# Performance work log

Measured on AMD Instinct MI355X. Metric: run time of the kernel, lower is better.

Reference implementation:

```python
import jax, jax.numpy as jnp
import numpy as np
import math

B, S, D = 8, 1024, 1024
NH, NKV, HD = 16, 8, 64
BLK_NUM, BLK_SIZE = 128, 8

def apply_rope(x, cos, sin):
    # x: (B,S,H,HD); cos/sin: (S, HD//2)
    x1 = x[..., 0::2]
    x2 = x[..., 1::2]
    c = cos[None, :, None, :]
    s = sin[None, :, None, :]
    r1 = x1 * c - x2 * s
    r2 = x1 * s + x2 * c
    out = jnp.stack([r1, r2], axis=-1).reshape(x.shape)
    return out

def setup_inputs() -> dict:
    key = jax.random.key(0)
    ks = jax.random.split(key, 7)
    x = jax.random.normal(ks[0], (B, S, D), dtype=jnp.float32)
    scale = 1.0 / math.sqrt(D)
    wq = jax.random.normal(ks[1], (D, NH * HD), dtype=jnp.float32) * scale
    wk = jax.random.normal(ks[2], (D, NKV * HD), dtype=jnp.float32) * scale
    wv = jax.random.normal(ks[3], (D, NKV * HD), dtype=jnp.float32) * scale
    wo = jax.random.normal(ks[4], (NH * HD, D), dtype=jnp.float32) * scale
    pos = jnp.arange(S, dtype=jnp.float32)
    inv_freq = 1.0 / (10000.0 ** (jnp.arange(0, HD, 2, dtype=jnp.float32) / HD))
    ang = pos[:, None] * inv_freq[None, :]
    freqs_cis_cos = jnp.cos(ang)
    freqs_cis_sin = jnp.sin(ang)
    return {"x": x, "wq": wq, "wk": wk, "wv": wv, "wo": wo,
            "freqs_cis_cos": freqs_cis_cos, "freqs_cis_sin": freqs_cis_sin,
            "start_pos": 0}

def reference(x, wq, wk, wv, wo, freqs_cis_cos, freqs_cis_sin, start_pos):
    q = (x @ wq).reshape(B, S, NH, HD)
    k = (x @ wk).reshape(B, S, NKV, HD)
    v = (x @ wv).reshape(B, S, NKV, HD)
    q = apply_rope(q, freqs_cis_cos, freqs_cis_sin)
    k = apply_rope(k, freqs_cis_cos, freqs_cis_sin)
    # GQA: repeat kv heads
    rep = NH // NKV
    k = jnp.repeat(k, rep, axis=2)  # (B,S,NH,HD)
    v = jnp.repeat(v, rep, axis=2)
    # block-causal mask: q in block i attends to kv blocks j <= i
    blk_id = jnp.arange(S) // BLK_SIZE
    mask = blk_id[:, None] >= blk_id[None, :]  # (S,S)
    scores = jnp.einsum('bqhd,bkhd->bhqk', q, k) / math.sqrt(HD)
    scores = jnp.where(mask[None, None], scores, -jnp.inf)
    attn = jax.nn.softmax(scores, axis=-1)
    out = jnp.einsum('bhqk,bkhd->bqhd', attn, v).reshape(B, S, NH * HD)
    return out @ wo
```

## Files before the change

### kernel.cpp

```cpp
#include <hip/hip_runtime.h>
#include <cstdint>
#include <math.h>

#define B_   8
#define S_   1024
#define D_   1024
#define NH_  16
#define NKV_ 8
#define HD_  64
#define M_   (B_*S_)

using bf16   = __bf16;
using bf16x4 = __attribute__((ext_vector_type(4))) __bf16;
using bf16x8 = __attribute__((ext_vector_type(8))) __bf16;
using f32x4  = __attribute__((ext_vector_type(4))) float;

__device__ __forceinline__ void gll16(const bf16* g, const bf16* l) {
    __builtin_amdgcn_global_load_lds(
        (const __attribute__((address_space(1))) unsigned int*)(uintptr_t)g,
        (__attribute__((address_space(3))) unsigned int*)(uintptr_t)l,
        16, 0, 0);
}

__device__ __forceinline__ void vm_wait0()  { asm volatile("s_waitcnt vmcnt(0)" ::: "memory"); }
__device__ __forceinline__ void bar()       { __builtin_amdgcn_s_barrier(); asm volatile("" ::: "memory"); }

__global__ void k_prep1(const float* __restrict__ x,
                        const float* __restrict__ wq, const float* __restrict__ wk,
                        const float* __restrict__ wv, const float* __restrict__ wo,
                        bf16* __restrict__ xb, bf16* __restrict__ wqkvT, bf16* __restrict__ woT) {
    __shared__ float tile[64 * 65];
    int bid = blockIdx.x;
    int t = threadIdx.x;
    if (bid < 8192) {
        int i = bid * 256 + t;
        float4 v = ((const float4*)x)[i];
        bf16x4 o = { (bf16)v.x, (bf16)v.y, (bf16)v.z, (bf16)v.w };
        ((bf16x4*)xb)[i] = o;
        return;
    }
    int b2 = bid - 8192;
    int bx = b2 % 48, by = b2 / 48;
    const int R = 1024;
    const float* in; bf16* out; int C, xo;
    if (bx < 16)      { in = wq; out = wqkvT;               C = 1024; xo = bx; }
    else if (bx < 24) { in = wk; out = wqkvT + 1024 * 1024; C = 512;  xo = bx - 16; }
    else if (bx < 32) { in = wv; out = wqkvT + 1536 * 1024; C = 512;  xo = bx - 24; }
    else              { in = wo; out = woT;                 C = 1024; xo = bx - 32; }
    int r0 = by * 64, c0 = xo * 64;
    #pragma unroll
    for (int it = 0; it < 16; ++it) {
        int idx = it * 256 + t;
        int r = idx >> 6, c = idx & 63;
        tile[r * 65 + c] = in[(size_t)(r0 + r) * C + c0 + c];
    }
    __syncthreads();
    #pragma unroll
    for (int it = 0; it < 16; ++it) {
        int idx = it * 256 + t;
        int c = idx >> 6, r = idx & 63;
        out[(size_t)(c0 + c) * R + r0 + r] = (bf16)tile[r * 65 + c];
    }
}

template <typename OutT, int BN>
__global__ __launch_bounds__(512, 2) void k_gemm256(const bf16* __restrict__ A,
                                                    const bf16* __restrict__ Bt,
                                                    OutT* __restrict__ C, int M, int N, int K) {
    constexpr int NI = BN / 64;
    constexpr int NB = (BN * 8) / 512;
    __shared__ __align__(16) bf16 aLds[2 * 256 * 64];
    __shared__ __align__(16) bf16 bLds[2 * BN * 64];
    const int t    = threadIdx.x;
    const int lane = t & 63;
    const int w    = t >> 6;
    const int quad = lane >> 4;
    const int l16  = lane & 15;
    const int wr   = w >> 2;
    const int wc   = w & 3;

    int bid = blockIdx.y * gridDim.x + blockIdx.x;
    int cpx = (gridDim.x * gridDim.y) >> 3;
    int sw  = (bid & 7) * cpx + (bid >> 3);
    int bx  = sw % gridDim.x, by = sw / gridDim.x;
    const int m0 = by * 256;
    const int n0 = bx * BN;

    f32x4 acc[8][NI] = {};

    auto stageA = [&](int kb, int buf) {
        const int k0 = kb << 6;
        #pragma unroll
        for (int it = 0; it < 4; ++it) {
            int ci = it * 512 + t;
            int r = ci >> 3, c = ci & 7;
            int cg = c ^ (r & 7);
            gll16(A + (size_t)(m0 + r) * K + k0 + cg * 8, aLds + buf * (256 * 64) + ci * 8);
        }
    };
    auto stageB = [&](int kb, int buf) {
        const int k0 = kb << 6;
        #pragma unroll
        for (int it = 0; it < NB; ++it) {
            int ci = it * 512 + t;
            int r = ci >> 3, c = ci & 7;
            int cg = c ^ (r & 7);
            gll16(Bt + (size_t)(n0 + r) * K + k0 + cg * 8, bLds + buf * (BN * 64) + ci * 8);
        }
    };

    const int NT = K >> 6;

    auto phase = [&](int buf, int kk, int mh, int stageSel, int nkb, bool lastInTile) {
        const bf16* aL = aLds + buf * (256 * 64);
        const bf16* bL = bLds + buf * (BN * 64);
        bf16x8 af[4], bfr[NI];
        #pragma unroll
        for (int i = 0; i < 4; ++i) {
            int row = wr * 128 + (mh * 4 + i) * 16 + l16;
            int ch  = (kk * 4 + quad) ^ (row & 7);
            af[i] = *(const bf16x8*)&aL[row * 64 + ch * 8];
        }
        #pragma unroll
        for (int ni = 0; ni < NI; ++ni) {
            int row = wc * (NI * 16) + ni * 16 + l16;
            int ch  = (kk * 4 + quad) ^ (row & 7);
            bfr[ni] = *(const bf16x8*)&bL[row * 64 + ch * 8];
        }
        if (stageSel == 1) stageA(nkb, buf ^ 1);
        else if (stageSel == 2) stageB(nkb, buf ^ 1);
        bar();
        __builtin_amdgcn_s_setprio(1);
        #pragma unroll
        for (int i = 0; i < 4; ++i)
            #pragma unroll
            for (int ni = 0; ni < NI; ++ni)
                acc[mh * 4 + i][ni] = __builtin_amdgcn_mfma_f32_16x16x32_bf16(af[i], bfr[ni], acc[mh * 4 + i][ni], 0, 0, 0);
        __builtin_amdgcn_s_setprio(0);
        if (lastInTile) vm_wait0();
        bar();
    };

    auto doTile = [&](int T, int buf) {
        bool hn = (T + 1 < NT);
        phase(buf, 0, 0, hn ? 1 : 0, T + 1, false);
        phase(buf, 0, 1, hn ? 2 : 0, T + 1, false);
        phase(buf, 1, 0, 0, 0, false);
        phase(buf, 1, 1, 0, 0, true);
    };

    stageA(0, 0); stageB(0, 0);
    vm_wait0();
    bar();
    for (int T = 0; T < NT; T += 2) {
        doTile(T, 0);
        doTile(T + 1, 1);
    }

    #pragma unroll
    for (int mi = 0; mi < 8; ++mi)
        #pragma unroll
        for (int ni = 0; ni < NI; ++ni)
            #pragma unroll
            for (int r = 0; r < 4; ++r) {
                int row = m0 + wr * 128 + mi * 16 + quad * 4 + r;
                int col = n0 + wc * (NI * 16) + ni * 16 + l16;
                C[(size_t)row * N + col] = (OutT)acc[mi][ni][r];
            }
}

__global__ void k_prep2(const bf16* __restrict__ qkv, const float* __restrict__ cosg,
                        const float* __restrict__ sing, bf16* __restrict__ qd,
                        bf16* __restrict__ kd, bf16* __restrict__ vt) {
    __shared__ __align__(16) bf16 tile[64 * 72];
    int bid = blockIdx.x;
    int t = threadIdx.x;
    if (bid < 8192) {
        if (t < 192) {
            int token = bid;
            int b = token >> 10, s = token & 1023;
            int hh = t >> 3, i8 = t & 7;
            float4 c4 = *(const float4*)&cosg[s * 32 + i8 * 4];
            float4 s4 = *(const float4*)&sing[s * 32 + i8 * 4];
            int srcBase, dstBase;
            bf16* dst;
            float sf;
            if (hh < 16) {
                srcBase = token * 2048 + hh * 64;
                dstBase = ((b * NH_ + hh) * S_ + s) * 64;
                dst = qd;
                sf = 0.180336879f;
            } else {
                int h = hh - 16;
                srcBase = token * 2048 + 1024 + h * 64;
                dstBase = ((b * NKV_ + h) * S_ + s) * 64;
                dst = kd;
                sf = 1.0f;
            }
            bf16x8 v = *(const bf16x8*)&qkv[srcBase + i8 * 8];
            const float cc[4] = { c4.x, c4.y, c4.z, c4.w };
            const float ss[4] = { s4.x, s4.y, s4.z, s4.w };
            bf16x8 o;
            #pragma unroll
            for (int j = 0; j < 4; ++j) {
                float e  = (float)v[2 * j];
                float od = (float)v[2 * j + 1];
                o[2 * j]     = (bf16)(sf * (e * cc[j] - od * ss[j]));
                o[2 * j + 1] = (bf16)(sf * (e * ss[j] + od * cc[j]));
            }
            *(bf16x8*)&dst[dstBase + i8 * 8] = o;
        }
        return;
    }
    int b2 = bid - 8192;
    int st = b2 & 15;
    int h  = (b2 >> 4) & 7;
    int b  = b2 >> 7;
    int s0 = st * 64;
    #pragma unroll
    for (int it = 0; it < 2; ++it) {
        int ci = it * 256 + t;
        int r = ci >> 3, c = ci & 7;
        *(uint4*)&tile[r * 72 + c * 8] =
            *(const uint4*)&qkv[(size_t)(b * S_ + s0 + r) * 2048 + 1536 + h * 64 + c * 8];
    }
    __syncthreads();
    #pragma unroll
    for (int it = 0; it < 2; ++it) {
        int ci = it * 256 + t;
        int d = ci >> 3, sc = ci & 7;
        int g = sc >> 2, q4 = sc & 3;
        bf16x8 v;
        #pragma unroll
        for (int j = 0; j < 8; ++j) {
            int s_ext = g * 32 + q4 * 4 + (j & 3) + 16 * (j >> 2);
            v[j] = tile[s_ext * 72 + d];
        }
        *(bf16x8*)&vt[(size_t)((b * NKV_ + h) * 64 + d) * S_ + s0 + sc * 8] = v;
    }
}

__global__ __launch_bounds__(256) void k_attn(const bf16* __restrict__ q, const bf16* __restrict__ k,
                                              const bf16* __restrict__ vt, bf16* __restrict__ out) {
    __shared__ __align__(16) bf16 kt[2 * 64 * 64];
    __shared__ __align__(16) bf16 vtt[2 * 64 * 64];
    int bid = blockIdx.x;
    int qt = 15 - (bid >> 7);
    int combo = bid & 127;
    int b = combo >> 4, h = combo & 15;
    int hkv = h >> 1;
    int t = threadIdx.x;
    int w = t >> 6, lane = t & 63, quad = lane >> 4, l16 = lane & 15;

    const bf16* qh = q + (size_t)(b * NH_ + h) * S_ * 64;
    int qw = qt * 64 + w * 16;
    const bf16* qb = qh + (size_t)(qw + l16) * 64;
    bf16x8 qf0 = *(const bf16x8*)(qb + quad * 8);
    bf16x8 qf1 = *(const bf16x8*)(qb + 32 + quad * 8);

    const bf16* kg = k  + (size_t)(b * NKV_ + hkv) * S_ * 64;
    const bf16* vg = vt + (size_t)(b * NKV_ + hkv) * 64 * S_;

    const int sr0 = t >> 3;
    const int cs  = t & 7;

    auto stage = [&](int u, int buf) {
        int k0 = u * 64;
        #pragma unroll
        for (int it = 0; it < 2; ++it) {
            int r  = sr0 + it * 32;
            int cg = cs ^ (r & 7);
            int ci = it * 256 + t;
            gll16(kg + (size_t)(k0 + r) * 64 + cg * 8, kt  + buf * 4096 + ci * 8);
            gll16(vg + (size_t)r * S_ + k0 + cg * 8,   vtt + buf * 4096 + ci * 8);
        }
    };

    const bf16 one = (bf16)1.0f;
    const bf16x8 vones = { one, one, one, one, one, one, one, one };

    f32x4 o[4] = {};
    f32x4 ol = {};
    const int klim = ((qw + l16) & ~7) + 8;

    auto unit = [&](int u, int buf, bool diag) {
        const bf16* ktb = kt  + buf * 4096;
        const bf16* vtb = vtt + buf * 4096;
        int k0 = u * 64;

        f32x4 sc[4] = {};
        #pragma unroll
        for (int kk = 0; kk < 2; ++kk)
            #pragma unroll
            for (int f = 0; f < 4; ++f) {
                int row = f * 16 + l16;
                int ch  = (kk * 4 + quad) ^ (row & 7);
                bf16x8 af = *(const bf16x8*)&ktb[row * 64 + ch * 8];
                sc[f] = __builtin_amdgcn_mfma_f32_16x16x32_bf16(af, kk ? qf1 : qf0, sc[f], 0, 0, 0);
            }

        float p[4][4];
        #pragma unroll
        for (int f = 0; f < 4; ++f)
            #pragma unroll
            for (int r = 0; r < 4; ++r) {
                float pv = __builtin_amdgcn_exp2f(sc[f][r]);
                if (diag && (k0 + f * 16 + quad * 4 + r >= klim)) pv = 0.f;
                p[f][r] = pv;
            }

        bf16x8 pa0, pa1;
        #pragma unroll
        for (int j = 0; j < 4; ++j) {
            pa0[j]     = (bf16)p[0][j];
            pa0[j + 4] = (bf16)p[1][j];
            pa1[j]     = (bf16)p[2][j];
            pa1[j + 4] = (bf16)p[3][j];
        }

        ol = __builtin_amdgcn_mfma_f32_16x16x32_bf16(pa0, vones, ol, 0, 0, 0);
        ol = __builtin_amdgcn_mfma_f32_16x16x32_bf16(pa1, vones, ol, 0, 0, 0);

        #pragma unroll
        for (int dc = 0; dc < 4; ++dc) {
            int row = dc * 16 + l16;
            #pragma unroll
            for (int kk = 0; kk < 2; ++kk) {
                int ch = (kk * 4 + quad) ^ (row & 7);
                bf16x8 vb = *(const bf16x8*)&vtb[row * 64 + ch * 8];
                o[dc] = __builtin_amdgcn_mfma_f32_16x16x32_bf16(kk ? pa1 : pa0, vb, o[dc], 0, 0, 0);
            }
        }
        vm_wait0();
        bar();
    };

    const int NU = qt + 1;
    stage(0, 0);
    vm_wait0();
    bar();

    int u = 0;
    for (; u + 2 <= NU; u += 2) {
        stage(u + 1, 1);
        unit(u, 0, false);
        if (u + 2 < NU) stage(u + 2, 0);
        unit(u + 1, 1, (u + 1) == NU - 1);
    }
    if (u < NU) unit(u, 0, true);

    #pragma unroll
    for (int r = 0; r < 4; ++r) {
        float invl = 1.0f / ol[r];
        #pragma unroll
        for (int dc = 0; dc < 4; ++dc) {
            int row = qw + quad * 4 + r;
            int col = h * 64 + dc * 16 + l16;
            out[(size_t)(b * S_ + row) * 1024 + col] = (bf16)(o[dc][r] * invl);
        }
    }
}

extern "C" void kernel_launch(void* const* d_in, const int* in_sizes, int n_in,
                              void* d_out, int out_size, void* d_ws, size_t ws_size,
                              hipStream_t stream) {
    const float* x  = (const float*)d_in[0];
    const float* wq = (const float*)d_in[1];
    const float* wk = (const float*)d_in[2];
    const float* wv = (const float*)d_in[3];
    const float* wo = (const float*)d_in[4];
    const float* fc = (const float*)d_in[5];
    const float* fs = (const float*)d_in[6];
    (void)in_sizes; (void)n_in; (void)out_size; (void)ws_size;

    char* ws = (char*)d_ws;
    bf16* xb    = (bf16*)(ws);
    bf16* wqkvT = (bf16*)(ws + (16u << 20));
    bf16* woT   = (bf16*)(ws + (20u << 20));
    bf16* qkvb  = (bf16*)(ws + (22u << 20));
    bf16* kb    = (bf16*)(ws + (54u << 20));
    bf16* vtb   = (bf16*)(ws + (62u << 20));
    bf16* qb    = xb;
    bf16* attnb = qkvb;

    k_prep1<<<dim3(8960), dim3(256), 0, stream>>>(x, wq, wk, wv, wo, xb, wqkvT, woT);

    k_gemm256<bf16, 256><<<dim3(8, 32), dim3(512), 0, stream>>>(xb, wqkvT, qkvb, M_, 2048, 1024);

    k_prep2<<<dim3(9216), dim3(256), 0, stream>>>(qkvb, fc, fs, qb, kb, vtb);

    k_attn<<<dim3(2048), dim3(256), 0, stream>>>(qb, kb, vtb, attnb);

    k_gemm256<float, 128><<<dim3(8, 32), dim3(512), 0, stream>>>(attnb, woT, (float*)d_out, M_, 1024, 1024);
}
```

Measured before the change: 207.1 us.

## Triple-buffer GEMM K-tiles with counted vmcnt waits and 2x4 wave layout

Rewrites the shared GEMM kernel to use a 3-stage LDS ring with prefetch two tiles ahead, replacing wait-all with partial vmcnt waits so global loads overlap more compute. The block tile is fixed at 256x128 with waves arranged 4x2 (64x64 per wave), so the QKV projection now launches twice as many blocks instead of using a 256-wide N tile. LDS use grows to 144KB per block, which may limit residency to one block per CU despite the launch bounds, and each wave's A/B fragment reuse changes.

```diff
diff --git a/kernel.cpp b/kernel.cpp
--- a/kernel.cpp
+++ b/kernel.cpp
@@ -22,7 +22,9 @@
         16, 0, 0);
 }
 
-__device__ __forceinline__ void vm_wait0()  { asm volatile("s_waitcnt vmcnt(0)" ::: "memory"); }
+__device__ __forceinline__ void vm_wait0()  { asm volatile("s_waitcnt vmcnt(0)"  ::: "memory"); }
+__device__ __forceinline__ void vm_wait6()  { asm volatile("s_waitcnt vmcnt(6)"  ::: "memory"); }
+__device__ __forceinline__ void vm_wait12() { asm volatile("s_waitcnt vmcnt(12)" ::: "memory"); }
 __device__ __forceinline__ void bar()       { __builtin_amdgcn_s_barrier(); asm volatile("" ::: "memory"); }
 
 __global__ void k_prep1(const float* __restrict__ x,
@@ -63,108 +65,98 @@
     }
 }
 
-template <typename OutT, int BN>
+template <typename OutT>
 __global__ __launch_bounds__(512, 2) void k_gemm256(const bf16* __restrict__ A,
                                                     const bf16* __restrict__ Bt,
                                                     OutT* __restrict__ C, int M, int N, int K) {
-    constexpr int NI = BN / 64;
-    constexpr int NB = (BN * 8) / 512;
-    __shared__ __align__(16) bf16 aLds[2 * 256 * 64];
-    __shared__ __align__(16) bf16 bLds[2 * BN * 64];
+    __shared__ __align__(16) bf16 aL3[3 * 256 * 64];
+    __shared__ __align__(16) bf16 bL3[3 * 128 * 64];
     const int t    = threadIdx.x;
     const int lane = t & 63;
     const int w    = t >> 6;
     const int quad = lane >> 4;
     const int l16  = lane & 15;
-    const int wr   = w >> 2;
-    const int wc   = w & 3;
+    const int wr   = w >> 1;
+    const int wc   = w & 1;
 
     int bid = blockIdx.y * gridDim.x + blockIdx.x;
     int cpx = (gridDim.x * gridDim.y) >> 3;
     int sw  = (bid & 7) * cpx + (bid >> 3);
     int bx  = sw % gridDim.x, by = sw / gridDim.x;
     const int m0 = by * 256;
-    const int n0 = bx * BN;
-
-    f32x4 acc[8][NI] = {};
-
-    auto stageA = [&](int kb, int buf) {
+    const int n0 = bx * 128;
+
+    f32x4 acc[4][4] = {};
+
+    auto stage = [&](int kb, int sbuf) {
         const int k0 = kb << 6;
         #pragma unroll
         for (int it = 0; it < 4; ++it) {
             int ci = it * 512 + t;
             int r = ci >> 3, c = ci & 7;
             int cg = c ^ (r & 7);
-            gll16(A + (size_t)(m0 + r) * K + k0 + cg * 8, aLds + buf * (256 * 64) + ci * 8);
-        }
-    };
-    auto stageB = [&](int kb, int buf) {
-        const int k0 = kb << 6;
-        #pragma unroll
-        for (int it = 0; it < NB; ++it) {
+            gll16(A + (size_t)(m0 + r) * K + k0 + cg * 8, aL3 + sbuf * (256 * 64) + ci * 8);
+        }
+        #pragma unroll
+        for (int it = 0; it < 2; ++it) {
             int ci = it * 512 + t;
             int r = ci >> 3, c = ci & 7;
             int cg = c ^ (r & 7);
-            gll16(Bt + (size_t)(n0 + r) * K + k0 + cg * 8, bLds + buf * (BN * 64) + ci * 8);
+            gll16(Bt + (size_t)(n0 + r) * K + k0 + cg * 8, bL3 + sbuf * (128 * 64) + ci * 8);
         }
     };
 
     const int NT = K >> 6;
 
-    auto phase = [&](int buf, int kk, int mh, int stageSel, int nkb, bool lastInTile) {
-        const bf16* aL = aLds + buf * (256 * 64);
-        const bf16* bL = bLds + buf * (BN * 64);
-        bf16x8 af[4], bfr[NI];
-        #pragma unroll
-        for (int i = 0; i < 4; ++i) {
-            int row = wr * 128 + (mh * 4 + i) * 16 + l16;
-            int ch  = (kk * 4 + quad) ^ (row & 7);
-            af[i] = *(const bf16x8*)&aL[row * 64 + ch * 8];
-        }
-        #pragma unroll
-        for (int ni = 0; ni < NI; ++ni) {
-            int row = wc * (NI * 16) + ni * 16 + l16;
-            int ch  = (kk * 4 + quad) ^ (row & 7);
-            bfr[ni] = *(const bf16x8*)&bL[row * 64 + ch * 8];
-        }
-        if (stageSel == 1) stageA(nkb, buf ^ 1);
-        else if (stageSel == 2) stageB(nkb, buf ^ 1);
+    auto doTile = [&](int T, int CUR, int STG) {
+        if (T + 2 < NT) { stage(T + 2, STG); vm_wait12(); }
+        else if (T + 1 < NT) vm_wait6();
+        else vm_wait0();
         bar();
-        __builtin_amdgcn_s_setprio(1);
-        #pragma unroll
-        for (int i = 0; i < 4; ++i)
-            #pragma unroll
-            for (int ni = 0; ni < NI; ++ni)
-                acc[mh * 4 + i][ni] = __builtin_amdgcn_mfma_f32_16x16x32_bf16(af[i], bfr[ni], acc[mh * 4 + i][ni], 0, 0, 0);
-        __builtin_amdgcn_s_setprio(0);
-        if (lastInTile) vm_wait0();
+        const bf16* aL = aL3 + CUR * (256 * 64);
+        const bf16* bL = bL3 + CUR * (128 * 64);
+        #pragma unroll
+        for (int kk = 0; kk < 2; ++kk) {
+            bf16x8 af[4], bfr[4];
+            #pragma unroll
+            for (int mi = 0; mi < 4; ++mi) {
+                int row = wr * 64 + mi * 16 + l16;
+                int ch  = (kk * 4 + quad) ^ (row & 7);
+                af[mi] = *(const bf16x8*)&aL[row * 64 + ch * 8];
+            }
+            #pragma unroll
+            for (int ni = 0; ni < 4; ++ni) {
+                int row = wc * 64 + ni * 16 + l16;
+                int ch  = (kk * 4 + quad) ^ (row & 7);
+                bfr[ni] = *(const bf16x8*)&bL[row * 64 + ch * 8];
+            }
+            __builtin_amdgcn_s_setprio(1);
+            #pragma unroll
+            for (int mi = 0; mi < 4; ++mi)
+                #pragma unroll
+                for (int ni = 0; ni < 4; ++ni)
+                    acc[mi][ni] = __builtin_amdgcn_mfma_f32_16x16x32_bf16(af[mi], bfr[ni], acc[mi][ni], 0, 0, 0);
+            __builtin_amdgcn_s_setprio(0);
+        }
         bar();
     };
 
-    auto doTile = [&](int T, int buf) {
-        bool hn = (T + 1 < NT);
-        phase(buf, 0, 0, hn ? 1 : 0, T + 1, false);
-        phase(buf, 0, 1, hn ? 2 : 0, T + 1, false);
-        phase(buf, 1, 0, 0, 0, false);
-        phase(buf, 1, 1, 0, 0, true);
-    };
-
-    stageA(0, 0); stageB(0, 0);
-    vm_wait0();
-    bar();
-    for (int T = 0; T < NT; T += 2) {
-        doTile(T, 0);
-        doTile(T + 1, 1);
-    }
-
-    #pragma unroll
-    for (int mi = 0; mi < 8; ++mi)
-        #pragma unroll
-        for (int ni = 0; ni < NI; ++ni)
+    stage(0, 0);
+    stage(1, 1);
+    for (int T = 0; T < NT; T += 3) {
+        doTile(T, 0, 2);
+        if (T + 1 < NT) doTile(T + 1, 1, 0);
+        if (T + 2 < NT) doTile(T + 2, 2, 1);
+    }
+
+    #pragma unroll
+    for (int mi = 0; mi < 4; ++mi)
+        #pragma unroll
+        for (int ni = 0; ni < 4; ++ni)
             #pragma unroll
             for (int r = 0; r < 4; ++r) {
-                int row = m0 + wr * 128 + mi * 16 + quad * 4 + r;
-                int col = n0 + wc * (NI * 16) + ni * 16 + l16;
+                int row = m0 + wr * 64 + mi * 16 + quad * 4 + r;
+                int col = n0 + wc * 64 + ni * 16 + l16;
                 C[(size_t)row * N + col] = (OutT)acc[mi][ni][r];
             }
 }
@@ -385,11 +377,11 @@
 
     k_prep1<<<dim3(8960), dim3(256), 0, stream>>>(x, wq, wk, wv, wo, xb, wqkvT, woT);
 
-    k_gemm256<bf16, 256><<<dim3(8, 32), dim3(512), 0, stream>>>(xb, wqkvT, qkvb, M_, 2048, 1024);
+    k_gemm256<bf16><<<dim3(16, 32), dim3(512), 0, stream>>>(xb, wqkvT, qkvb, M_, 2048, 1024);
 
     k_prep2<<<dim3(9216), dim3(256), 0, stream>>>(qkvb, fc, fs, qb, kb, vtb);
 
     k_attn<<<dim3(2048), dim3(256), 0, stream>>>(qb, kb, vtb, attnb);
 
-    k_gemm256<float, 128><<<dim3(8, 32), dim3(512), 0, stream>>>(attnb, woT, (float*)d_out, M_, 1024, 1024);
-}
+    k_gemm256<float><<<dim3(8, 32), dim3(512), 0, stream>>>(attnb, woT, (float*)d_out, M_, 1024, 1024);
+}
```

Measured after the change: 208.5 us. Within noise of the previous version (+0.7%).

## Restructure GEMM main loop into finer-grained prefetch with partial vmcnt waits

Applied to the files above, without the earlier changes.

Rewrites the bf16 GEMM kernel's K-loop into four quadrant sub-phases, each over both k-steps of a tile. Global-to-LDS staging of the next tiles is split into halves and issued earlier, up to two tiles ahead. The next buffer is partially prefilled, and waits use vmcnt(5/6) instead of vmcnt(0). It also remaps B rows so each wave's N columns split into two halves that can be staged independently. This aims to hide global load latency behind MFMA work. The cost is more complex buffer reuse that must stay race-free.

```diff
diff --git a/kernel.cpp b/kernel.cpp
--- a/kernel.cpp
+++ b/kernel.cpp
@@ -22,7 +22,9 @@
         16, 0, 0);
 }
 
-__device__ __forceinline__ void vm_wait0()  { asm volatile("s_waitcnt vmcnt(0)" ::: "memory"); }
+__device__ __forceinline__ void vm_wait0()  { asm volatile("s_waitcnt vmcnt(0)"  ::: "memory"); }
+__device__ __forceinline__ void vm_wait5()  { asm volatile("s_waitcnt vmcnt(5)"  ::: "memory"); }
+__device__ __forceinline__ void vm_wait6()  { asm volatile("s_waitcnt vmcnt(6)"  ::: "memory"); }
 __device__ __forceinline__ void bar()       { __builtin_amdgcn_s_barrier(); asm volatile("" ::: "memory"); }
 
 __global__ void k_prep1(const float* __restrict__ x,
@@ -63,14 +65,13 @@
     }
 }
 
-template <typename OutT, int BN>
-__global__ __launch_bounds__(512, 2) void k_gemm256(const bf16* __restrict__ A,
-                                                    const bf16* __restrict__ Bt,
-                                                    OutT* __restrict__ C, int M, int N, int K) {
-    constexpr int NI = BN / 64;
-    constexpr int NB = (BN * 8) / 512;
-    __shared__ __align__(16) bf16 aLds[2 * 256 * 64];
-    __shared__ __align__(16) bf16 bLds[2 * BN * 64];
+template <typename OutT, int NI>
+__global__ __launch_bounds__(512, 2) void k_gemm8p(const bf16* __restrict__ A,
+                                                   const bf16* __restrict__ Bt,
+                                                   OutT* __restrict__ C, int M, int N, int K) {
+    constexpr int BN = NI * 64;
+    __shared__ __align__(16) bf16 aL2[2 * 256 * 64];
+    __shared__ __align__(16) bf16 bL2[2 * BN * 64];
     const int t    = threadIdx.x;
     const int lane = t & 63;
     const int w    = t >> 6;
@@ -88,73 +89,108 @@
 
     f32x4 acc[8][NI] = {};
 
-    auto stageA = [&](int kb, int buf) {
+    auto stageA2 = [&](int kb, int dbuf, int itX, int itY) {
         const int k0 = kb << 6;
         #pragma unroll
-        for (int it = 0; it < 4; ++it) {
+        for (int u = 0; u < 2; ++u) {
+            int it = u ? itY : itX;
             int ci = it * 512 + t;
             int r = ci >> 3, c = ci & 7;
             int cg = c ^ (r & 7);
-            gll16(A + (size_t)(m0 + r) * K + k0 + cg * 8, aLds + buf * (256 * 64) + ci * 8);
-        }
-    };
-    auto stageB = [&](int kb, int buf) {
+            gll16(A + (size_t)(m0 + r) * K + k0 + cg * 8, aL2 + dbuf * (256 * 64) + ci * 8);
+        }
+    };
+    auto stageBh = [&](int kb, int dbuf, int nh) {
         const int k0 = kb << 6;
         #pragma unroll
-        for (int it = 0; it < NB; ++it) {
+        for (int j = 0; j < NI / 2; ++j) {
+            int it = nh * (NI / 2) + j;
             int ci = it * 512 + t;
-            int r = ci >> 3, c = ci & 7;
-            int cg = c ^ (r & 7);
-            gll16(Bt + (size_t)(n0 + r) * K + k0 + cg * 8, bLds + buf * (BN * 64) + ci * 8);
-        }
+            int lr = ci >> 3, cs = ci & 7;
+            int cg = cs ^ (lr & 7);
+            int idx = lr - nh * (BN / 2);
+            int wcc = idx / (NI * 8);
+            int off = idx % (NI * 8);
+            int g   = wcc * (NI * 16) + nh * (NI * 8) + off;
+            gll16(Bt + (size_t)(n0 + g) * K + k0 + cg * 8, bL2 + dbuf * (BN * 64) + ci * 8);
+        }
+    };
+
+    auto loadA = [&](const bf16* aL, int mh, bf16x8 (&af)[8]) {
+        #pragma unroll
+        for (int mi = 0; mi < 4; ++mi)
+            #pragma unroll
+            for (int kk = 0; kk < 2; ++kk) {
+                int row = wr * 128 + (mh * 4 + mi) * 16 + l16;
+                int ch  = (kk * 4 + quad) ^ (row & 7);
+                af[mi * 2 + kk] = *(const bf16x8*)&aL[row * 64 + ch * 8];
+            }
+    };
+    auto loadB = [&](const bf16* bL, int nh, bf16x8 (&bfr)[NI]) {
+        #pragma unroll
+        for (int j = 0; j < NI / 2; ++j)
+            #pragma unroll
+            for (int kk = 0; kk < 2; ++kk) {
+                int lr = nh * (BN / 2) + wc * (NI * 8) + j * 16 + l16;
+                int ch = (kk * 4 + quad) ^ (lr & 7);
+                bfr[j * 2 + kk] = *(const bf16x8*)&bL[lr * 64 + ch * 8];
+            }
+    };
+    auto mmac = [&](int mh, int nh, bf16x8 (&af)[8], bf16x8 (&bfr)[NI]) {
+        __builtin_amdgcn_s_setprio(1);
+        #pragma unroll
+        for (int mi = 0; mi < 4; ++mi)
+            #pragma unroll
+            for (int j = 0; j < NI / 2; ++j)
+                #pragma unroll
+                for (int kk = 0; kk < 2; ++kk)
+                    acc[mh * 4 + mi][nh * (NI / 2) + j] =
+                        __builtin_amdgcn_mfma_f32_16x16x32_bf16(af[mi * 2 + kk], bfr[j * 2 + kk],
+                                                                acc[mh * 4 + mi][nh * (NI / 2) + j], 0, 0, 0);
+        __builtin_amdgcn_s_setprio(0);
     };
 
     const int NT = K >> 6;
 
-    auto phase = [&](int buf, int kk, int mh, int stageSel, int nkb, bool lastInTile) {
-        const bf16* aL = aLds + buf * (256 * 64);
-        const bf16* bL = bLds + buf * (BN * 64);
-        bf16x8 af[4], bfr[NI];
-        #pragma unroll
-        for (int i = 0; i < 4; ++i) {
-            int row = wr * 128 + (mh * 4 + i) * 16 + l16;
-            int ch  = (kk * 4 + quad) ^ (row & 7);
-            af[i] = *(const bf16x8*)&aL[row * 64 + ch * 8];
-        }
-        #pragma unroll
-        for (int ni = 0; ni < NI; ++ni) {
-            int row = wc * (NI * 16) + ni * 16 + l16;
-            int ch  = (kk * 4 + quad) ^ (row & 7);
-            bfr[ni] = *(const bf16x8*)&bL[row * 64 + ch * 8];
-        }
-        if (stageSel == 1) stageA(nkb, buf ^ 1);
-        else if (stageSel == 2) stageB(nkb, buf ^ 1);
-        bar();
-        __builtin_amdgcn_s_setprio(1);
-        #pragma unroll
-        for (int i = 0; i < 4; ++i)
-            #pragma unroll
-            for (int ni = 0; ni < NI; ++ni)
-                acc[mh * 4 + i][ni] = __builtin_amdgcn_mfma_f32_16x16x32_bf16(af[i], bfr[ni], acc[mh * 4 + i][ni], 0, 0, 0);
-        __builtin_amdgcn_s_setprio(0);
-        if (lastInTile) vm_wait0();
-        bar();
-    };
-
-    auto doTile = [&](int T, int buf) {
-        bool hn = (T + 1 < NT);
-        phase(buf, 0, 0, hn ? 1 : 0, T + 1, false);
-        phase(buf, 0, 1, hn ? 2 : 0, T + 1, false);
-        phase(buf, 1, 0, 0, 0, false);
-        phase(buf, 1, 1, 0, 0, true);
-    };
-
-    stageA(0, 0); stageB(0, 0);
-    vm_wait0();
+    auto tile = [&](int T, int bufc) {
+        const bf16* aL = aL2 + bufc * (256 * 64);
+        const bf16* bL = bL2 + bufc * (BN * 64);
+        bf16x8 af[8], bfr[NI];
+        loadA(aL, 0, af); loadB(bL, 0, bfr);
+        if (T + 1 < NT) stageBh(T + 1, bufc ^ 1, 1);
+        bar();
+        mmac(0, 0, af, bfr);
+        bar();
+        loadB(bL, 1, bfr);
+        if (T + 2 < NT) stageA2(T + 2, bufc, 0, 2);
+        bar();
+        mmac(0, 1, af, bfr);
+        bar();
+        loadA(aL, 1, af); loadB(bL, 0, bfr);
+        bar();
+        mmac(1, 0, af, bfr);
+        bar();
+        loadB(bL, 1, bfr);
+        if (T + 2 < NT) {
+            stageA2(T + 2, bufc, 1, 3);
+            stageBh(T + 2, bufc, 0);
+            if constexpr (NI == 4) vm_wait6(); else vm_wait5();
+        } else {
+            vm_wait0();
+        }
+        bar();
+        mmac(1, 1, af, bfr);
+        bar();
+    };
+
+    stageA2(0, 0, 0, 2); stageA2(0, 0, 1, 3); stageBh(0, 0, 0); stageBh(0, 0, 1);
+    stageA2(1, 1, 0, 2); stageA2(1, 1, 1, 3); stageBh(1, 1, 0);
+    if constexpr (NI == 4) vm_wait6(); else vm_wait5();
     bar();
+
     for (int T = 0; T < NT; T += 2) {
-        doTile(T, 0);
-        doTile(T + 1, 1);
+        tile(T, 0);
+        tile(T + 1, 1);
     }
 
     #pragma unroll
@@ -385,11 +421,11 @@
 
     k_prep1<<<dim3(8960), dim3(256), 0, stream>>>(x, wq, wk, wv, wo, xb, wqkvT, woT);
 
-    k_gemm256<bf16, 256><<<dim3(8, 32), dim3(512), 0, stream>>>(xb, wqkvT, qkvb, M_, 2048, 1024);
+    k_gemm8p<bf16, 4><<<dim3(8, 32), dim3(512), 0, stream>>>(xb, wqkvT, qkvb, M_, 2048, 1024);
 
     k_prep2<<<dim3(9216), dim3(256), 0, stream>>>(qkvb, fc, fs, qb, kb, vtb);
 
     k_attn<<<dim3(2048), dim3(256), 0, stream>>>(qb, kb, vtb, attnb);
 
-    k_gemm256<float, 128><<<dim3(8, 32), dim3(512), 0, stream>>>(attnb, woT, (float*)d_out, M_, 1024, 1024);
-}
+    k_gemm8p<float, 2><<<dim3(8, 32), dim3(512), 0, stream>>>(attnb, woT, (float*)d_out, M_, 1024, 1024);
+}
```

After: 202.8 us. 1.02x faster.
